# Kernel tuning notes

Hardware: AMD Instinct MI355X
Metric: run time of the kernel (lower is better)

## Reference

```python
import jax, jax.numpy as jnp
import numpy as np

T, I, H, O, M = 1024, 128, 512, 512, 32768
BETA = 8.0


def setup_inputs() -> dict:
    key = jax.random.key(0)
    ks = jax.random.split(key, 8)
    s = 0.05  # small init scale to keep tanh unsaturated
    return {
        "inp": jax.random.normal(ks[0], (T, I), jnp.float32),
        "x_obs": jax.nn.softmax(jax.random.normal(ks[1], (T, O), jnp.float32), axis=-1),
        "patterns": jax.random.normal(ks[2], (M, O + H), jnp.float32),  # stored [x | g] slots
        "last_hidden": jnp.zeros((H,), jnp.float32),
        "W_ih": jax.random.normal(ks[3], (H, I), jnp.float32) * s,
        "W_hh": jax.random.normal(ks[4], (H, H), jnp.float32) * s,
        "b_ih": jax.random.normal(ks[5], (H,), jnp.float32) * s,
        "b_hh": jax.random.normal(ks[6], (H,), jnp.float32) * s,
    }


def _retrieve(query, keys, values, beta):
    # distance-based slot attention: softmax(-beta * ||q - k||^2) @ values
    # sqdist via the expanded form to avoid a [T, M, D] intermediate
    d = (jnp.sum(query * query, axis=-1, keepdims=True)
         + jnp.sum(keys * keys, axis=-1)[None, :]
         - 2.0 * query @ keys.T)  # [T, M]
    w = jax.nn.softmax(-beta * d, axis=-1)
    return w @ values  # [T, O]


def reference(inp, x_obs, patterns, last_hidden, W_ih, W_hh, b_ih, b_hh):
    # single-layer tanh RNN (nn.RNN semantics), unbatched [T, I]
    def step(h, x):
        h_new = jnp.tanh(x @ W_ih.T + b_ih + h @ W_hh.T + b_hh)
        return h_new, h_new

    h_last, g_cur = jax.lax.scan(step, last_hidden, inp)  # g_cur: [T, H]

    x_vals = patterns[:, :O]   # stored x-parts
    g_keys = patterns[:, O:]   # stored g-parts
    prob_g = _retrieve(g_cur, g_keys, x_vals, BETA)   # index_g=True
    prob_x = _retrieve(x_obs, x_vals, x_vals, BETA)   # index_g=False
    # memory.store(hstack([x_obs, g_cur])) is a pure side effect on the buffer
    # and does not affect this step's outputs.
    return prob_g, prob_x, g_cur, h_last[None, :]
```

## Files before the change

kernel.cpp:

```cpp
#include <hip/hip_runtime.h>
#include <math.h>

#define T_STEPS 1024
#define I_DIM   128
#define H_DIM   512
#define O_DIM   512
#define M_PAT   32768
#define SCAN_ROLES 32
#define VT_STR  32800

typedef __attribute__((ext_vector_type(8))) short s16x8;
typedef __attribute__((ext_vector_type(4))) float f32x4;

__device__ __forceinline__ void bf_split(float f, unsigned short& hi, unsigned short& lo) {
  unsigned u = __builtin_bit_cast(unsigned, f);
  hi = (unsigned short)(u >> 16);
  float r = f - __builtin_bit_cast(float, u & 0xFFFF0000u);
  lo = (unsigned short)(__builtin_bit_cast(unsigned, r) >> 16);
}
__device__ __forceinline__ unsigned short f2bf(float f) {
  return (unsigned short)(__builtin_bit_cast(unsigned, f) >> 16);
}
__device__ __forceinline__ float bf2f(unsigned short b) {
  return __builtin_bit_cast(float, ((unsigned)b) << 16);
}

__global__ __launch_bounds__(256) void xw_kernel(const float* __restrict__ inp,
    const float* __restrict__ W_ih, const float* __restrict__ b_ih,
    const float* __restrict__ b_hh, float* __restrict__ xw) {
  int t = blockIdx.x;
  __shared__ float4 xs4[I_DIM / 4];
  if (threadIdx.x < I_DIM / 4)
    xs4[threadIdx.x] = ((const float4*)(inp + (size_t)t * I_DIM))[threadIdx.x];
  __syncthreads();
  for (int j = threadIdx.x; j < H_DIM; j += 256) {
    const float4* w4 = (const float4*)(W_ih + (size_t)j * I_DIM);
    float acc = 0.f;
#pragma unroll
    for (int i = 0; i < I_DIM / 4; i++) {
      float4 w = w4[i]; float4 x = xs4[i];
      acc += w.x * x.x + w.y * x.y + w.z * x.z + w.w * x.w;
    }
    xw[(size_t)t * H_DIM + j] = acc + b_ih[j] + b_hh[j];
  }
}

__global__ __launch_bounds__(64, 1) void scan_kernel(
    const float* __restrict__ W_hh, const float* __restrict__ xw,
    const float* __restrict__ h0, float* __restrict__ g_cur,
    float* __restrict__ h_last, unsigned* __restrict__ sync,
    unsigned* __restrict__ henc) {
  unsigned* cnt  = sync + 64;
  unsigned* dec  = sync + 128;
  __shared__ int role_s;
  if (threadIdx.x == 0) {
    unsigned xcd = __builtin_amdgcn_s_getreg(6164) & 7u;
    unsigned my_idx = __hip_atomic_fetch_add(&cnt[xcd], 1u, __ATOMIC_ACQ_REL,
                                             __HIP_MEMORY_SCOPE_AGENT);
    if (blockIdx.x == 0) {
      int chosen = -1;
      while (chosen < 0) {
        for (int x = 0; x < 8; x++)
          if (__hip_atomic_load(&cnt[x], __ATOMIC_ACQUIRE,
                                __HIP_MEMORY_SCOPE_AGENT) >= (unsigned)SCAN_ROLES) {
            chosen = x; break;
          }
        if (chosen < 0) __builtin_amdgcn_s_sleep(2);
      }
      __hip_atomic_store(dec, 1u + (unsigned)chosen, __ATOMIC_RELEASE,
                         __HIP_MEMORY_SCOPE_AGENT);
    }
    unsigned d;
    while ((d = __hip_atomic_load(dec, __ATOMIC_ACQUIRE,
                                  __HIP_MEMORY_SCOPE_AGENT)) == 0u)
      __builtin_amdgcn_s_sleep(2);
    role_s = (xcd == d - 1u && my_idx < (unsigned)SCAN_ROLES) ? (int)my_idx : -1;
  }
  __syncthreads();
  const int role = role_s;
  if (role < 0) return;

  const int lane = threadIdx.x;
  const int g    = lane & 3;
  const int row  = role * 16 + (lane >> 2);

  float4 w[32];
  const float4* wsrc = (const float4*)(W_hh + (size_t)row * H_DIM + g * 128);
#pragma unroll
  for (int i = 0; i < 32; i++) w[i] = wsrc[i];
#pragma unroll
  for (int i = 0; i < 32; i++) {
    asm volatile("" : "+v"(w[i].x), "+v"(w[i].y), "+v"(w[i].z), "+v"(w[i].w));
  }

  __shared__ float hbuf[528];

  float xw_next = xw[row];

  for (int t = 0; t < T_STEPS; t++) {
    float xwv = xw_next;
    if (t + 1 < T_STEPS)
      xw_next = xw[(size_t)(t + 1) * H_DIM + row];

    if (t == 0) {
#pragma unroll
      for (int j = 0; j < 8; j++) {
        int c = 64 * j + lane;
        hbuf[c + 4 * (j >> 1)] = h0[c];
      }
    } else {
      const unsigned* src = henc + (size_t)(t - 1) * H_DIM;
      unsigned u[8];
#pragma unroll
      for (int j = 0; j < 8; j++)
        u[j] = __hip_atomic_load(src + 64 * j + lane, __ATOMIC_RELAXED,
                                 __HIP_MEMORY_SCOPE_AGENT);
      bool again = true;
      while (again) {
        again = false;
#pragma unroll
        for (int j = 0; j < 8; j++)
          if (__builtin_bit_cast(float, u[j]) < 1.0f) {
            again = true;
            u[j] = __hip_atomic_load(src + 64 * j + lane, __ATOMIC_RELAXED,
                                     __HIP_MEMORY_SCOPE_AGENT);
          }
      }
#pragma unroll
      for (int j = 0; j < 8; j++) {
        int c = 64 * j + lane;
        hbuf[c + 4 * (j >> 1)] = __builtin_bit_cast(float, u[j]) - 2.0f;
      }
    }
    asm volatile("s_waitcnt lgkmcnt(0)" ::: "memory");

    const float4* hb = (const float4*)&hbuf[g * 132];
    float a0 = 0.f, a1 = 0.f, a2 = 0.f, a3 = 0.f;
#pragma unroll
    for (int i = 0; i < 8; i++) {
      float4 x0 = hb[4 * i], x1 = hb[4 * i + 1], x2 = hb[4 * i + 2], x3 = hb[4 * i + 3];
      float4 w0 = w[4 * i], w1 = w[4 * i + 1], w2 = w[4 * i + 2], w3 = w[4 * i + 3];
      a0 += x0.x * w0.x + x0.y * w0.y + x0.z * w0.z + x0.w * w0.w;
      a1 += x1.x * w1.x + x1.y * w1.y + x1.z * w1.z + x1.w * w1.w;
      a2 += x2.x * w2.x + x2.y * w2.y + x2.z * w2.z + x2.w * w2.w;
      a3 += x3.x * w3.x + x3.y * w3.y + x3.z * w3.z + x3.w * w3.w;
    }
    float a = (a0 + a1) + (a2 + a3);
    a += __shfl_xor(a, 1, 4);
    a += __shfl_xor(a, 2, 4);

    if (g == 0) {
      float pre = a + xwv;
      float e = __expf(2.f * pre);
      float h = 1.f - 2.f / (e + 1.f);
      __hip_atomic_store(henc + (size_t)t * H_DIM + row,
                         __builtin_bit_cast(unsigned, h + 2.0f),
                         __ATOMIC_RELAXED, __HIP_MEMORY_SCOPE_AGENT);
      g_cur[(size_t)t * H_DIM + row] = h;
      if (t == T_STEPS - 1) h_last[row] = h;
    }
  }
}

__global__ __launch_bounds__(256) void norms_kernel(const float* __restrict__ patterns,
    float* __restrict__ bkx, float* __restrict__ bkg) {
  int lane = threadIdx.x & 63;
  int m = blockIdx.x * 4 + (threadIdx.x >> 6);
  const float4* row = (const float4*)(patterns + (size_t)m * (O_DIM + H_DIM));
  float ax = 0.f, ag = 0.f;
#pragma unroll
  for (int jj = 0; jj < 4; jj++) {
    float4 v = row[lane + 64 * jj];
    float s = v.x * v.x + v.y * v.y + v.z * v.z + v.w * v.w;
    if (jj < 2) ax += s; else ag += s;
  }
#pragma unroll
  for (int off = 1; off < 64; off <<= 1) {
    ax += __shfl_xor(ax, off, 64);
    ag += __shfl_xor(ag, off, 64);
  }
  if (lane == 0) { bkx[m] = 8.f * ax; bkg[m] = 8.f * ag; }
}

__global__ __launch_bounds__(256) void vt_kernel(const float* __restrict__ patterns,
                                                 unsigned short* __restrict__ Vt) {
  __shared__ unsigned short tile[64 * 68];
  int kt = blockIdx.x;
  int vt = blockIdx.y;
#pragma unroll
  for (int i = 0; i < 4; i++) {
    int f = threadIdx.x + 256 * i;
    int key = f >> 4, c4 = f & 15;
    float4 v = *(const float4*)(patterns + (size_t)(kt * 64 + key) * 1024 + vt * 64 + c4 * 4);
    unsigned short* dst = &tile[key * 68 + c4 * 4];
    dst[0] = f2bf(v.x); dst[1] = f2bf(v.y); dst[2] = f2bf(v.z); dst[3] = f2bf(v.w);
  }
  __syncthreads();
  int vd = threadIdx.x >> 2, q4 = threadIdx.x & 3;
  unsigned short tmp[16];
#pragma unroll
  for (int k = 0; k < 16; k++) tmp[k] = tile[(q4 * 16 + k) * 68 + vd];
  size_t ob = (size_t)(vt * 64 + vd) * VT_STR + kt * 64 + q4 * 16;
#pragma unroll
  for (int h = 0; h < 2; h++) {
    s16x8 pk;
#pragma unroll
    for (int j = 0; j < 8; j++) pk[j] = (short)tmp[h * 8 + j];
    *(s16x8*)&Vt[ob + h * 8] = pk;
  }
}

template <bool USE_VT>
__global__ __launch_bounds__(512, 2) void flash_kernel(
    const float* __restrict__ Qg, const float* __restrict__ Qx,
    const float* __restrict__ patterns, const float* __restrict__ bkx,
    const float* __restrict__ bkg, const unsigned short* __restrict__ Vt,
    float* __restrict__ pacc, float* __restrict__ pml, int S) {
  const int bid  = blockIdx.x;
  const int sidx = bid >> 6;
  const int ret  = (bid >> 5) & 1;
  const int qt   = bid & 31;
  const int qbase = qt * 32;

  const float* Qp  = ret ? Qx : Qg;
  const float* Kp  = patterns + (ret ? 0 : O_DIM);
  const float* bkk = ret ? bkx : bkg;

  const int chunk = M_PAT / S;
  const int kbeg = sidx * chunk, kend = kbeg + chunk;

  const int lane = threadIdx.x & 63;
  const int wid  = threadIdx.x >> 6;
  const int qg   = wid >> 2;
  const int kw   = wid & 3;
  const int quad = lane >> 4;
  const int l16  = lane & 15;

  __shared__ unsigned short stage_u16[16384];
  __shared__ unsigned short p_lds[32 * 72];
  __shared__ float mrow_s[32], lrow_s[32], alpha_s[32];
  __shared__ int flag_s;

  const int qrow = qbase + qg * 16 + l16;
  s16x8 qhi[16], qlo[16];
#pragma unroll
  for (int kst = 0; kst < 16; kst++) {
    const float4* src = (const float4*)(Qp + (size_t)qrow * 512 + kst * 32 + quad * 8);
    float4 a = src[0], b = src[1];
    float fv[8] = {a.x, a.y, a.z, a.w, b.x, b.y, b.z, b.w};
    s16x8 h, l;
#pragma unroll
    for (int j = 0; j < 8; j++) {
      unsigned short hb, lb; bf_split(fv[j], hb, lb);
      h[j] = (short)hb; l[j] = (short)lb;
    }
    qhi[kst] = h; qlo[kst] = l;
  }

  if (threadIdx.x < 32) { mrow_s[threadIdx.x] = -INFINITY; lrow_s[threadIdx.x] = 0.f; }

  f32x4 o[8];
#pragma unroll
  for (int nb = 0; nb < 8; nb++) o[nb] = (f32x4){0.f, 0.f, 0.f, 0.f};
  float ov[32];
  if (!USE_VT) {
#pragma unroll
    for (int j = 0; j < 32; j++) ov[j] = 0.f;
  }
  const int row2 = threadIdx.x >> 4;
  const int c0   = threadIdx.x & 15;

  for (int k0 = kbeg; k0 < kend; k0 += 64) {
    f32x4 sc = (f32x4){0.f, 0.f, 0.f, 0.f};
#pragma unroll
    for (int dc = 0; dc < 4; dc++) {
      __syncthreads();
      if (dc == 0 && threadIdx.x == 0) flag_s = 0;
#pragma unroll
      for (int i = 0; i < 2; i++) {
        int oid = threadIdx.x + 512 * i;
        int key = oid >> 4, oct = oid & 15;
        const float4* src = (const float4*)(Kp + (size_t)(k0 + key) * 1024 + dc * 128 + oct * 8);
        float4 a = src[0], b = src[1];
        float fv[8] = {a.x, a.y, a.z, a.w, b.x, b.y, b.z, b.w};
        s16x8 hv, lv;
#pragma unroll
        for (int j = 0; j < 8; j++) {
          unsigned short hb, lb; bf_split(fv[j], hb, lb);
          hv[j] = (short)hb; lv[j] = (short)lb;
        }
        int base = (key * 16 + (oct ^ (key & 7))) * 8;
        *(s16x8*)&stage_u16[base] = hv;
        *(s16x8*)&stage_u16[8192 + base] = lv;
      }
      __syncthreads();
#pragma unroll
      for (int ks = 0; ks < 4; ks++) {
        int kst = dc * 4 + ks;
        int key = kw * 16 + l16;
        int oct = ks * 4 + quad;
        int base = (key * 16 + (oct ^ (key & 7))) * 8;
        s16x8 kh = *(const s16x8*)&stage_u16[base];
        s16x8 kl = *(const s16x8*)&stage_u16[8192 + base];
        sc = __builtin_amdgcn_mfma_f32_16x16x32_bf16(qhi[kst], kh, sc, 0, 0, 0);
        sc = __builtin_amdgcn_mfma_f32_16x16x32_bf16(qlo[kst], kh, sc, 0, 0, 0);
        sc = __builtin_amdgcn_mfma_f32_16x16x32_bf16(qhi[kst], kl, sc, 0, 0, 0);
      }
    }
    float bkv = bkk[k0 + kw * 16 + l16];
    __syncthreads();
    float* S_f = (float*)stage_u16;
#pragma unroll
    for (int r = 0; r < 4; r++)
      S_f[(qg * 16 + quad * 4 + r) * 68 + kw * 16 + l16] = 16.f * sc[r] - bkv;
    __syncthreads();

    float s4[4], p4[4];
#pragma unroll
    for (int c = 0; c < 4; c++) s4[c] = S_f[row2 * 68 + c0 + 16 * c];
    float tmax = fmaxf(fmaxf(s4[0], s4[1]), fmaxf(s4[2], s4[3]));
#pragma unroll
    for (int off = 1; off < 16; off <<= 1) tmax = fmaxf(tmax, __shfl_xor(tmax, off, 16));
    float mold = mrow_s[row2];
    float mnew = fmaxf(mold, tmax);
    float tsum = 0.f;
#pragma unroll
    for (int c = 0; c < 4; c++) { p4[c] = __expf(s4[c] - mnew); tsum += p4[c]; }
#pragma unroll
    for (int off = 1; off < 16; off <<= 1) tsum += __shfl_xor(tsum, off, 16);
#pragma unroll
    for (int c = 0; c < 4; c++) p_lds[row2 * 72 + c0 + 16 * c] = f2bf(p4[c]);
    if (c0 == 0) {
      float al = __expf(mold - mnew);
      alpha_s[row2] = al;
      mrow_s[row2] = mnew;
      lrow_s[row2] = lrow_s[row2] * al + tsum;
      if (tmax > mold - 25.f) flag_s = 1;
    }
    __syncthreads();
    const int doPV = flag_s;

    if (doPV) {
      if (USE_VT) {
        float alr[4];
#pragma unroll
        for (int r = 0; r < 4; r++) alr[r] = alpha_s[qg * 16 + quad * 4 + r];
#pragma unroll
        for (int nb = 0; nb < 8; nb++) {
          o[nb][0] *= alr[0]; o[nb][1] *= alr[1]; o[nb][2] *= alr[2]; o[nb][3] *= alr[3];
        }
#pragma unroll
        for (int ks2 = 0; ks2 < 2; ks2++) {
          s16x8 pf = *(const s16x8*)&p_lds[(qg * 16 + l16) * 72 + ks2 * 32 + quad * 8];
#pragma unroll
          for (int nb = 0; nb < 8; nb++) {
            int vd = kw * 128 + nb * 16 + l16;
            s16x8 vf = *(const s16x8*)(Vt + (size_t)vd * VT_STR + (k0 + ks2 * 32 + quad * 8));
            o[nb] = __builtin_amdgcn_mfma_f32_16x16x32_bf16(pf, vf, o[nb], 0, 0, 0);
          }
        }
      } else {
        float al = alpha_s[row2];
#pragma unroll
        for (int j = 0; j < 32; j++) ov[j] *= al;
        for (int key = 0; key < 64; key++) {
          float w = bf2f(p_lds[row2 * 72 + key]);
          const float4* vsrc = (const float4*)(patterns + (size_t)(k0 + key) * 1024 + c0 * 32);
#pragma unroll
          for (int j = 0; j < 8; j++) {
            float4 v = vsrc[j];
            ov[4 * j + 0] += w * v.x; ov[4 * j + 1] += w * v.y;
            ov[4 * j + 2] += w * v.z; ov[4 * j + 3] += w * v.w;
          }
        }
      }
    }
  }

  __syncthreads();
  size_t pbase = ((size_t)(ret * S + sidx) * T_STEPS + qbase);
  if (USE_VT) {
#pragma unroll
    for (int nb = 0; nb < 8; nb++)
#pragma unroll
      for (int r = 0; r < 4; r++)
        pacc[(pbase + qg * 16 + quad * 4 + r) * 512 + kw * 128 + nb * 16 + l16] = o[nb][r];
  } else {
#pragma unroll
    for (int j = 0; j < 32; j++)
      pacc[(pbase + row2) * 512 + c0 * 32 + j] = ov[j];
  }
  if (threadIdx.x < 32) {
    pml[(pbase + threadIdx.x) * 2]     = mrow_s[threadIdx.x];
    pml[(pbase + threadIdx.x) * 2 + 1] = lrow_s[threadIdx.x];
  }
}

__global__ __launch_bounds__(256) void combine_kernel(
    const float* __restrict__ pacc, const float* __restrict__ pml,
    float* __restrict__ out, int S) {
  int b = blockIdx.x;
  int ret = b >> 10, r = b & 1023;
  float M = -INFINITY;
  for (int s = 0; s < S; s++)
    M = fmaxf(M, pml[((size_t)(ret * S + s) * T_STEPS + r) * 2]);
  float L = 0.f;
  for (int s = 0; s < S; s++) {
    size_t mb = ((size_t)(ret * S + s) * T_STEPS + r) * 2;
    L += pml[mb + 1] * __expf(pml[mb] - M);
  }
  float inv = 1.0f / L;
  for (int cc = threadIdx.x; cc < 512; cc += 256) {
    float acc = 0.f;
    for (int s = 0; s < S; s++) {
      size_t mb = ((size_t)(ret * S + s) * T_STEPS + r) * 2;
      float sc = __expf(pml[mb] - M);
      acc += sc * pacc[((size_t)(ret * S + s) * T_STEPS + r) * 512 + cc];
    }
    out[(size_t)ret * (T_STEPS * O_DIM) + (size_t)r * 512 + cc] = acc * inv;
  }
}

extern "C" void kernel_launch(void* const* d_in, const int* in_sizes, int n_in,
                              void* d_out, int out_size, void* d_ws, size_t ws_size,
                              hipStream_t stream) {
  const float* inp      = (const float*)d_in[0];
  const float* x_obs    = (const float*)d_in[1];
  const float* patterns = (const float*)d_in[2];
  const float* h0       = (const float*)d_in[3];
  const float* W_ih     = (const float*)d_in[4];
  const float* W_hh     = (const float*)d_in[5];
  const float* b_ih     = (const float*)d_in[6];
  const float* b_hh     = (const float*)d_in[7];

  float* out    = (float*)d_out;
  float* g_cur  = out + 1048576;
  float* h_last = out + 1572864;

  char* wsb = (char*)d_ws;
  size_t off = 0;
  auto alloc = [&](size_t bytes) -> char* {
    char* p = wsb + off; off += (bytes + 255) & ~(size_t)255; return p;
  };
  unsigned* sync = (unsigned*)alloc(8192);
  unsigned* henc = (unsigned*)alloc((size_t)T_STEPS * H_DIM * 4);
  float* xw  = (float*)alloc((size_t)T_STEPS * H_DIM * 4);
  float* bkx = (float*)alloc((size_t)M_PAT * 4);
  float* bkg = (float*)alloc((size_t)M_PAT * 4);
  size_t base = off;

  const size_t vt_bytes = (size_t)512 * VT_STR * 2;
  auto pml_bytes  = [](int S) { return (size_t)2 * S * T_STEPS * 2 * 4; };
  auto pacc_bytes = [](int S) { return (size_t)2 * S * T_STEPS * 512 * 4; };

  int S = 4; bool use_vt = false;
  if (base + pml_bytes(4) + pacc_bytes(4) + vt_bytes + 1024 <= ws_size) { S = 4; use_vt = true; }
  else if (base + pml_bytes(2) + pacc_bytes(2) + vt_bytes + 1024 <= ws_size) { S = 2; use_vt = true; }
  else if (base + pml_bytes(4) + pacc_bytes(4) + 1024 <= ws_size) { S = 4; use_vt = false; }
  else if (base + pml_bytes(2) + pacc_bytes(2) + 1024 <= ws_size) { S = 2; use_vt = false; }
  else { S = 1; use_vt = false; }

  float* pml  = (float*)alloc(pml_bytes(S));
  float* pacc = (float*)alloc(pacc_bytes(S));
  unsigned short* Vt = use_vt ? (unsigned short*)alloc(vt_bytes) : (unsigned short*)nullptr;

  hipMemsetAsync(sync, 0, 8192, stream);
  hipMemsetAsync(henc, 0, (size_t)T_STEPS * H_DIM * 4, stream);
  xw_kernel<<<T_STEPS, 256, 0, stream>>>(inp, W_ih, b_ih, b_hh, xw);
  scan_kernel<<<1024, 64, 0, stream>>>(W_hh, xw, h0, g_cur, h_last, sync, henc);
  norms_kernel<<<M_PAT / 4, 256, 0, stream>>>(patterns, bkx, bkg);
  if (use_vt) {
    vt_kernel<<<dim3(512, 8), 256, 0, stream>>>(patterns, Vt);
    flash_kernel<true><<<S * 64, 512, 0, stream>>>(g_cur, x_obs, patterns, bkx, bkg,
                                                   Vt, pacc, pml, S);
  } else {
    flash_kernel<false><<<S * 64, 512, 0, stream>>>(g_cur, x_obs, patterns, bkx, bkg,
                                                    nullptr, pacc, pml, S);
  }
  combine_kernel<<<2 * T_STEPS, 256, 0, stream>>>(pacc, pml, out, S);
}
```

Measured before the change: 2.624 ms.

## Fuse RNN scan with flash retrieval so attention overlaps the recurrence

Merges the scan kernel and the flash retrieval kernel into one persistent launch. The 32 scan workgroups run on one XCD, while the other workgroups pull work units from an atomic counter. x_obs retrieval units come first, and g units spin on the per-row henc readiness flags before they start. The goal is to hide the serial recurrence latency behind the independent attention work. The change also raises the key-split count S to as much as 16 for finer-grained units. The risks are spin-waiting that occupies compute units, larger combine and partial buffers, and possible contention between the flash waves and the latency-critical scan waves on the shared XCD.

```diff
diff --git a/kernel.cpp b/kernel.cpp
--- a/kernel.cpp
+++ b/kernel.cpp
@@ -45,14 +45,76 @@
   }
 }
 
-__global__ __launch_bounds__(64, 1) void scan_kernel(
+__global__ __launch_bounds__(256) void norms_kernel(const float* __restrict__ patterns,
+    float* __restrict__ bkx, float* __restrict__ bkg) {
+  int lane = threadIdx.x & 63;
+  int m = blockIdx.x * 4 + (threadIdx.x >> 6);
+  const float4* row = (const float4*)(patterns + (size_t)m * (O_DIM + H_DIM));
+  float ax = 0.f, ag = 0.f;
+#pragma unroll
+  for (int jj = 0; jj < 4; jj++) {
+    float4 v = row[lane + 64 * jj];
+    float s = v.x * v.x + v.y * v.y + v.z * v.z + v.w * v.w;
+    if (jj < 2) ax += s; else ag += s;
+  }
+#pragma unroll
+  for (int off = 1; off < 64; off <<= 1) {
+    ax += __shfl_xor(ax, off, 64);
+    ag += __shfl_xor(ag, off, 64);
+  }
+  if (lane == 0) { bkx[m] = 8.f * ax; bkg[m] = 8.f * ag; }
+}
+
+__global__ __launch_bounds__(256) void vt_kernel(const float* __restrict__ patterns,
+                                                 unsigned short* __restrict__ Vt) {
+  __shared__ unsigned short tile[64 * 68];
+  int kt = blockIdx.x;
+  int vt = blockIdx.y;
+#pragma unroll
+  for (int i = 0; i < 4; i++) {
+    int f = threadIdx.x + 256 * i;
+    int key = f >> 4, c4 = f & 15;
+    float4 v = *(const float4*)(patterns + (size_t)(kt * 64 + key) * 1024 + vt * 64 + c4 * 4);
+    unsigned short* dst = &tile[key * 68 + c4 * 4];
+    dst[0] = f2bf(v.x); dst[1] = f2bf(v.y); dst[2] = f2bf(v.z); dst[3] = f2bf(v.w);
+  }
+  __syncthreads();
+  int vd = threadIdx.x >> 2, q4 = threadIdx.x & 3;
+  unsigned short tmp[16];
+#pragma unroll
+  for (int k = 0; k < 16; k++) tmp[k] = tile[(q4 * 16 + k) * 68 + vd];
+  size_t ob = (size_t)(vt * 64 + vd) * VT_STR + kt * 64 + q4 * 16;
+#pragma unroll
+  for (int h = 0; h < 2; h++) {
+    s16x8 pk;
+#pragma unroll
+    for (int j = 0; j < 8; j++) pk[j] = (short)tmp[h * 8 + j];
+    *(s16x8*)&Vt[ob + h * 8] = pk;
+  }
+}
+
+template <bool USE_VT>
+__global__ __launch_bounds__(512, 2) void fused_kernel(
     const float* __restrict__ W_hh, const float* __restrict__ xw,
     const float* __restrict__ h0, float* __restrict__ g_cur,
     float* __restrict__ h_last, unsigned* __restrict__ sync,
-    unsigned* __restrict__ henc) {
+    unsigned* __restrict__ henc,
+    const float* __restrict__ Qx, const float* __restrict__ patterns,
+    const float* __restrict__ bkx, const float* __restrict__ bkg,
+    const unsigned short* __restrict__ Vt,
+    float* __restrict__ pacc, float* __restrict__ pml, int S) {
   unsigned* cnt  = sync + 64;
   unsigned* dec  = sync + 128;
+  unsigned* wctr = sync + 192;
+
   __shared__ int role_s;
+  __shared__ float hbuf[528];
+  __shared__ unsigned short stage_u16[16384];
+  __shared__ unsigned short p_lds[32 * 72];
+  __shared__ float mrow_s[32], lrow_s[32], alpha_s[32];
+  __shared__ int flag_s;
+  __shared__ int unit_s;
+
   if (threadIdx.x == 0) {
     unsigned xcd = __builtin_amdgcn_s_getreg(6164) & 7u;
     unsigned my_idx = __hip_atomic_fetch_add(&cnt[xcd], 1u, __ATOMIC_ACQ_REL,
@@ -74,160 +136,95 @@
     while ((d = __hip_atomic_load(dec, __ATOMIC_ACQUIRE,
                                   __HIP_MEMORY_SCOPE_AGENT)) == 0u)
       __builtin_amdgcn_s_sleep(2);
-    role_s = (xcd == d - 1u && my_idx < (unsigned)SCAN_ROLES) ? (int)my_idx : -1;
+    if (xcd == d - 1u) role_s = (my_idx < (unsigned)SCAN_ROLES) ? (int)my_idx : -2;
+    else               role_s = -1;
   }
   __syncthreads();
   const int role = role_s;
-  if (role < 0) return;
-
-  const int lane = threadIdx.x;
-  const int g    = lane & 3;
-  const int row  = role * 16 + (lane >> 2);
-
-  float4 w[32];
-  const float4* wsrc = (const float4*)(W_hh + (size_t)row * H_DIM + g * 128);
-#pragma unroll
-  for (int i = 0; i < 32; i++) w[i] = wsrc[i];
-#pragma unroll
-  for (int i = 0; i < 32; i++) {
-    asm volatile("" : "+v"(w[i].x), "+v"(w[i].y), "+v"(w[i].z), "+v"(w[i].w));
-  }
-
-  __shared__ float hbuf[528];
-
-  float xw_next = xw[row];
-
-  for (int t = 0; t < T_STEPS; t++) {
-    float xwv = xw_next;
-    if (t + 1 < T_STEPS)
-      xw_next = xw[(size_t)(t + 1) * H_DIM + row];
-
-    if (t == 0) {
-#pragma unroll
-      for (int j = 0; j < 8; j++) {
-        int c = 64 * j + lane;
-        hbuf[c + 4 * (j >> 1)] = h0[c];
-      }
-    } else {
-      const unsigned* src = henc + (size_t)(t - 1) * H_DIM;
-      unsigned u[8];
-#pragma unroll
-      for (int j = 0; j < 8; j++)
-        u[j] = __hip_atomic_load(src + 64 * j + lane, __ATOMIC_RELAXED,
-                                 __HIP_MEMORY_SCOPE_AGENT);
-      bool again = true;
-      while (again) {
-        again = false;
+  if (role == -2) return;
+
+  if (role >= 0) {
+    if (threadIdx.x >= 64) return;
+    const int lane = threadIdx.x;
+    const int g    = lane & 3;
+    const int row  = role * 16 + (lane >> 2);
+
+    float4 w[32];
+    const float4* wsrc = (const float4*)(W_hh + (size_t)row * H_DIM + g * 128);
+#pragma unroll
+    for (int i = 0; i < 32; i++) w[i] = wsrc[i];
+#pragma unroll
+    for (int i = 0; i < 32; i++) {
+      asm volatile("" : "+v"(w[i].x), "+v"(w[i].y), "+v"(w[i].z), "+v"(w[i].w));
+    }
+
+    float xw_next = xw[row];
+
+    for (int t = 0; t < T_STEPS; t++) {
+      float xwv = xw_next;
+      if (t + 1 < T_STEPS)
+        xw_next = xw[(size_t)(t + 1) * H_DIM + row];
+
+      if (t == 0) {
+#pragma unroll
+        for (int j = 0; j < 8; j++) {
+          int c = 64 * j + lane;
+          hbuf[c + 4 * (j >> 1)] = h0[c];
+        }
+      } else {
+        const unsigned* src = henc + (size_t)(t - 1) * H_DIM;
+        unsigned u[8];
 #pragma unroll
         for (int j = 0; j < 8; j++)
-          if (__builtin_bit_cast(float, u[j]) < 1.0f) {
-            again = true;
-            u[j] = __hip_atomic_load(src + 64 * j + lane, __ATOMIC_RELAXED,
-                                     __HIP_MEMORY_SCOPE_AGENT);
-          }
-      }
-#pragma unroll
-      for (int j = 0; j < 8; j++) {
-        int c = 64 * j + lane;
-        hbuf[c + 4 * (j >> 1)] = __builtin_bit_cast(float, u[j]) - 2.0f;
-      }
-    }
-    asm volatile("s_waitcnt lgkmcnt(0)" ::: "memory");
-
-    const float4* hb = (const float4*)&hbuf[g * 132];
-    float a0 = 0.f, a1 = 0.f, a2 = 0.f, a3 = 0.f;
-#pragma unroll
-    for (int i = 0; i < 8; i++) {
-      float4 x0 = hb[4 * i], x1 = hb[4 * i + 1], x2 = hb[4 * i + 2], x3 = hb[4 * i + 3];
-      float4 w0 = w[4 * i], w1 = w[4 * i + 1], w2 = w[4 * i + 2], w3 = w[4 * i + 3];
-      a0 += x0.x * w0.x + x0.y * w0.y + x0.z * w0.z + x0.w * w0.w;
-      a1 += x1.x * w1.x + x1.y * w1.y + x1.z * w1.z + x1.w * w1.w;
-      a2 += x2.x * w2.x + x2.y * w2.y + x2.z * w2.z + x2.w * w2.w;
-      a3 += x3.x * w3.x + x3.y * w3.y + x3.z * w3.z + x3.w * w3.w;
-    }
-    float a = (a0 + a1) + (a2 + a3);
-    a += __shfl_xor(a, 1, 4);
-    a += __shfl_xor(a, 2, 4);
-
-    if (g == 0) {
-      float pre = a + xwv;
-      float e = __expf(2.f * pre);
-      float h = 1.f - 2.f / (e + 1.f);
-      __hip_atomic_store(henc + (size_t)t * H_DIM + row,
-                         __builtin_bit_cast(unsigned, h + 2.0f),
-                         __ATOMIC_RELAXED, __HIP_MEMORY_SCOPE_AGENT);
-      g_cur[(size_t)t * H_DIM + row] = h;
-      if (t == T_STEPS - 1) h_last[row] = h;
-    }
-  }
-}
-
-__global__ __launch_bounds__(256) void norms_kernel(const float* __restrict__ patterns,
-    float* __restrict__ bkx, float* __restrict__ bkg) {
-  int lane = threadIdx.x & 63;
-  int m = blockIdx.x * 4 + (threadIdx.x >> 6);
-  const float4* row = (const float4*)(patterns + (size_t)m * (O_DIM + H_DIM));
-  float ax = 0.f, ag = 0.f;
-#pragma unroll
-  for (int jj = 0; jj < 4; jj++) {
-    float4 v = row[lane + 64 * jj];
-    float s = v.x * v.x + v.y * v.y + v.z * v.z + v.w * v.w;
-    if (jj < 2) ax += s; else ag += s;
-  }
-#pragma unroll
-  for (int off = 1; off < 64; off <<= 1) {
-    ax += __shfl_xor(ax, off, 64);
-    ag += __shfl_xor(ag, off, 64);
-  }
-  if (lane == 0) { bkx[m] = 8.f * ax; bkg[m] = 8.f * ag; }
-}
-
-__global__ __launch_bounds__(256) void vt_kernel(const float* __restrict__ patterns,
-                                                 unsigned short* __restrict__ Vt) {
-  __shared__ unsigned short tile[64 * 68];
-  int kt = blockIdx.x;
-  int vt = blockIdx.y;
-#pragma unroll
-  for (int i = 0; i < 4; i++) {
-    int f = threadIdx.x + 256 * i;
-    int key = f >> 4, c4 = f & 15;
-    float4 v = *(const float4*)(patterns + (size_t)(kt * 64 + key) * 1024 + vt * 64 + c4 * 4);
-    unsigned short* dst = &tile[key * 68 + c4 * 4];
-    dst[0] = f2bf(v.x); dst[1] = f2bf(v.y); dst[2] = f2bf(v.z); dst[3] = f2bf(v.w);
-  }
-  __syncthreads();
-  int vd = threadIdx.x >> 2, q4 = threadIdx.x & 3;
-  unsigned short tmp[16];
-#pragma unroll
-  for (int k = 0; k < 16; k++) tmp[k] = tile[(q4 * 16 + k) * 68 + vd];
-  size_t ob = (size_t)(vt * 64 + vd) * VT_STR + kt * 64 + q4 * 16;
-#pragma unroll
-  for (int h = 0; h < 2; h++) {
-    s16x8 pk;
-#pragma unroll
-    for (int j = 0; j < 8; j++) pk[j] = (short)tmp[h * 8 + j];
-    *(s16x8*)&Vt[ob + h * 8] = pk;
-  }
-}
-
-template <bool USE_VT>
-__global__ __launch_bounds__(512, 2) void flash_kernel(
-    const float* __restrict__ Qg, const float* __restrict__ Qx,
-    const float* __restrict__ patterns, const float* __restrict__ bkx,
-    const float* __restrict__ bkg, const unsigned short* __restrict__ Vt,
-    float* __restrict__ pacc, float* __restrict__ pml, int S) {
-  const int bid  = blockIdx.x;
-  const int sidx = bid >> 6;
-  const int ret  = (bid >> 5) & 1;
-  const int qt   = bid & 31;
-  const int qbase = qt * 32;
-
-  const float* Qp  = ret ? Qx : Qg;
-  const float* Kp  = patterns + (ret ? 0 : O_DIM);
-  const float* bkk = ret ? bkx : bkg;
-
-  const int chunk = M_PAT / S;
-  const int kbeg = sidx * chunk, kend = kbeg + chunk;
+          u[j] = __hip_atomic_load(src + 64 * j + lane, __ATOMIC_RELAXED,
+                                   __HIP_MEMORY_SCOPE_AGENT);
+        bool again = true;
+        while (again) {
+          again = false;
+#pragma unroll
+          for (int j = 0; j < 8; j++)
+            if (__builtin_bit_cast(float, u[j]) < 1.0f) {
+              again = true;
+              u[j] = __hip_atomic_load(src + 64 * j + lane, __ATOMIC_RELAXED,
+                                       __HIP_MEMORY_SCOPE_AGENT);
+            }
+        }
+#pragma unroll
+        for (int j = 0; j < 8; j++) {
+          int c = 64 * j + lane;
+          hbuf[c + 4 * (j >> 1)] = __builtin_bit_cast(float, u[j]) - 2.0f;
+        }
+      }
+      asm volatile("s_waitcnt lgkmcnt(0)" ::: "memory");
+
+      const float4* hb = (const float4*)&hbuf[g * 132];
+      float a0 = 0.f, a1 = 0.f, a2 = 0.f, a3 = 0.f;
+#pragma unroll
+      for (int i = 0; i < 8; i++) {
+        float4 x0 = hb[4 * i], x1 = hb[4 * i + 1], x2 = hb[4 * i + 2], x3 = hb[4 * i + 3];
+        float4 w0 = w[4 * i], w1 = w[4 * i + 1], w2 = w[4 * i + 2], w3 = w[4 * i + 3];
+        a0 += x0.x * w0.x + x0.y * w0.y + x0.z * w0.z + x0.w * w0.w;
+        a1 += x1.x * w1.x + x1.y * w1.y + x1.z * w1.z + x1.w * w1.w;
+        a2 += x2.x * w2.x + x2.y * w2.y + x2.z * w2.z + x2.w * w2.w;
+        a3 += x3.x * w3.x + x3.y * w3.y + x3.z * w3.z + x3.w * w3.w;
+      }
+      float a = (a0 + a1) + (a2 + a3);
+      a += __shfl_xor(a, 1, 4);
+      a += __shfl_xor(a, 2, 4);
+
+      if (g == 0) {
+        float pre = a + xwv;
+        float e = __expf(2.f * pre);
+        float h = 1.f - 2.f / (e + 1.f);
+        __hip_atomic_store(henc + (size_t)t * H_DIM + row,
+                           __builtin_bit_cast(unsigned, h + 2.0f),
+                           __ATOMIC_RELAXED, __HIP_MEMORY_SCOPE_AGENT);
+        g_cur[(size_t)t * H_DIM + row] = h;
+        if (t == T_STEPS - 1) h_last[row] = h;
+      }
+    }
+    return;
+  }
 
   const int lane = threadIdx.x & 63;
   const int wid  = threadIdx.x >> 6;
@@ -235,164 +232,197 @@
   const int kw   = wid & 3;
   const int quad = lane >> 4;
   const int l16  = lane & 15;
-
-  __shared__ unsigned short stage_u16[16384];
-  __shared__ unsigned short p_lds[32 * 72];
-  __shared__ float mrow_s[32], lrow_s[32], alpha_s[32];
-  __shared__ int flag_s;
-
-  const int qrow = qbase + qg * 16 + l16;
-  s16x8 qhi[16], qlo[16];
-#pragma unroll
-  for (int kst = 0; kst < 16; kst++) {
-    const float4* src = (const float4*)(Qp + (size_t)qrow * 512 + kst * 32 + quad * 8);
-    float4 a = src[0], b = src[1];
-    float fv[8] = {a.x, a.y, a.z, a.w, b.x, b.y, b.z, b.w};
-    s16x8 h, l;
-#pragma unroll
-    for (int j = 0; j < 8; j++) {
-      unsigned short hb, lb; bf_split(fv[j], hb, lb);
-      h[j] = (short)hb; l[j] = (short)lb;
-    }
-    qhi[kst] = h; qlo[kst] = l;
-  }
-
-  if (threadIdx.x < 32) { mrow_s[threadIdx.x] = -INFINITY; lrow_s[threadIdx.x] = 0.f; }
-
-  f32x4 o[8];
-#pragma unroll
-  for (int nb = 0; nb < 8; nb++) o[nb] = (f32x4){0.f, 0.f, 0.f, 0.f};
-  float ov[32];
-  if (!USE_VT) {
-#pragma unroll
-    for (int j = 0; j < 32; j++) ov[j] = 0.f;
-  }
   const int row2 = threadIdx.x >> 4;
   const int c0   = threadIdx.x & 15;
-
-  for (int k0 = kbeg; k0 < kend; k0 += 64) {
-    f32x4 sc = (f32x4){0.f, 0.f, 0.f, 0.f};
-#pragma unroll
-    for (int dc = 0; dc < 4; dc++) {
+  const int NU   = 64 * S;
+
+  for (;;) {
+    if (threadIdx.x == 0)
+      unit_s = (int)__hip_atomic_fetch_add(wctr, 1u, __ATOMIC_RELAXED,
+                                           __HIP_MEMORY_SCOPE_AGENT);
+    __syncthreads();
+    const int u = unit_s;
+    if (u >= NU) break;
+
+    int ret, qt, sidx;
+    if (u < 32 * S) { ret = 1; qt = u & 31; sidx = u >> 5; }
+    else { int v = u - 32 * S; qt = v / S; sidx = v - qt * S; ret = 0; }
+    const int qbase = qt * 32;
+
+    const float* Kp  = patterns + (ret ? 0 : O_DIM);
+    const float* bkk = ret ? bkx : bkg;
+    const int chunk = M_PAT / S;
+    const int kbeg = sidx * chunk, kend = kbeg + chunk;
+
+    const int qrow = qbase + qg * 16 + l16;
+    s16x8 qhi[16], qlo[16];
+#pragma unroll
+    for (int kst = 0; kst < 16; kst++) {
+      float fv[8];
+      if (ret) {
+        const float4* src = (const float4*)(Qx + (size_t)qrow * 512 + kst * 32 + quad * 8);
+        float4 a = src[0], b = src[1];
+        fv[0] = a.x; fv[1] = a.y; fv[2] = a.z; fv[3] = a.w;
+        fv[4] = b.x; fv[5] = b.y; fv[6] = b.z; fv[7] = b.w;
+      } else {
+        const unsigned* hs = henc + (size_t)qrow * H_DIM + kst * 32 + quad * 8;
+#pragma unroll
+        for (int j = 0; j < 8; j++) {
+          unsigned uv = __hip_atomic_load(hs + j, __ATOMIC_RELAXED,
+                                          __HIP_MEMORY_SCOPE_AGENT);
+          while (__builtin_bit_cast(float, uv) < 1.0f) {
+            __builtin_amdgcn_s_sleep(8);
+            uv = __hip_atomic_load(hs + j, __ATOMIC_RELAXED,
+                                   __HIP_MEMORY_SCOPE_AGENT);
+          }
+          fv[j] = __builtin_bit_cast(float, uv) - 2.0f;
+        }
+      }
+      s16x8 h, l;
+#pragma unroll
+      for (int j = 0; j < 8; j++) {
+        unsigned short hb, lb; bf_split(fv[j], hb, lb);
+        h[j] = (short)hb; l[j] = (short)lb;
+      }
+      qhi[kst] = h; qlo[kst] = l;
+    }
+
+    if (threadIdx.x < 32) { mrow_s[threadIdx.x] = -INFINITY; lrow_s[threadIdx.x] = 0.f; }
+
+    f32x4 o[8];
+#pragma unroll
+    for (int nb = 0; nb < 8; nb++) o[nb] = (f32x4){0.f, 0.f, 0.f, 0.f};
+    float ov[32];
+    if (!USE_VT) {
+#pragma unroll
+      for (int j = 0; j < 32; j++) ov[j] = 0.f;
+    }
+
+    for (int k0 = kbeg; k0 < kend; k0 += 64) {
+      f32x4 sc = (f32x4){0.f, 0.f, 0.f, 0.f};
+#pragma unroll
+      for (int dc = 0; dc < 4; dc++) {
+        __syncthreads();
+        if (dc == 0 && threadIdx.x == 0) flag_s = 0;
+#pragma unroll
+        for (int i = 0; i < 2; i++) {
+          int oid = threadIdx.x + 512 * i;
+          int key = oid >> 4, oct = oid & 15;
+          const float4* src = (const float4*)(Kp + (size_t)(k0 + key) * 1024 + dc * 128 + oct * 8);
+          float4 a = src[0], b = src[1];
+          float fv[8] = {a.x, a.y, a.z, a.w, b.x, b.y, b.z, b.w};
+          s16x8 hv, lv;
+#pragma unroll
+          for (int j = 0; j < 8; j++) {
+            unsigned short hb, lb; bf_split(fv[j], hb, lb);
+            hv[j] = (short)hb; lv[j] = (short)lb;
+          }
+          int base = (key * 16 + (oct ^ (key & 7))) * 8;
+          *(s16x8*)&stage_u16[base] = hv;
+          *(s16x8*)&stage_u16[8192 + base] = lv;
+        }
+        __syncthreads();
+#pragma unroll
+        for (int ks = 0; ks < 4; ks++) {
+          int kst = dc * 4 + ks;
+          int key = kw * 16 + l16;
+          int oct = ks * 4 + quad;
+          int base = (key * 16 + (oct ^ (key & 7))) * 8;
+          s16x8 kh = *(const s16x8*)&stage_u16[base];
+          s16x8 kl = *(const s16x8*)&stage_u16[8192 + base];
+          sc = __builtin_amdgcn_mfma_f32_16x16x32_bf16(qhi[kst], kh, sc, 0, 0, 0);
+          sc = __builtin_amdgcn_mfma_f32_16x16x32_bf16(qlo[kst], kh, sc, 0, 0, 0);
+          sc = __builtin_amdgcn_mfma_f32_16x16x32_bf16(qhi[kst], kl, sc, 0, 0, 0);
+        }
+      }
+      float bkv = bkk[k0 + kw * 16 + l16];
       __syncthreads();
-      if (dc == 0 && threadIdx.x == 0) flag_s = 0;
-#pragma unroll
-      for (int i = 0; i < 2; i++) {
-        int oid = threadIdx.x + 512 * i;
-        int key = oid >> 4, oct = oid & 15;
-        const float4* src = (const float4*)(Kp + (size_t)(k0 + key) * 1024 + dc * 128 + oct * 8);
-        float4 a = src[0], b = src[1];
-        float fv[8] = {a.x, a.y, a.z, a.w, b.x, b.y, b.z, b.w};
-        s16x8 hv, lv;
-#pragma unroll
-        for (int j = 0; j < 8; j++) {
-          unsigned short hb, lb; bf_split(fv[j], hb, lb);
-          hv[j] = (short)hb; lv[j] = (short)lb;
-        }
-        int base = (key * 16 + (oct ^ (key & 7))) * 8;
-        *(s16x8*)&stage_u16[base] = hv;
-        *(s16x8*)&stage_u16[8192 + base] = lv;
-      }
+      float* S_f = (float*)stage_u16;
+#pragma unroll
+      for (int r = 0; r < 4; r++)
+        S_f[(qg * 16 + quad * 4 + r) * 68 + kw * 16 + l16] = 16.f * sc[r] - bkv;
       __syncthreads();
-#pragma unroll
-      for (int ks = 0; ks < 4; ks++) {
-        int kst = dc * 4 + ks;
-        int key = kw * 16 + l16;
-        int oct = ks * 4 + quad;
-        int base = (key * 16 + (oct ^ (key & 7))) * 8;
-        s16x8 kh = *(const s16x8*)&stage_u16[base];
-        s16x8 kl = *(const s16x8*)&stage_u16[8192 + base];
-        sc = __builtin_amdgcn_mfma_f32_16x16x32_bf16(qhi[kst], kh, sc, 0, 0, 0);
-        sc = __builtin_amdgcn_mfma_f32_16x16x32_bf16(qlo[kst], kh, sc, 0, 0, 0);
-        sc = __builtin_amdgcn_mfma_f32_16x16x32_bf16(qhi[kst], kl, sc, 0, 0, 0);
-      }
-    }
-    float bkv = bkk[k0 + kw * 16 + l16];
+
+      float s4[4], p4[4];
+#pragma unroll
+      for (int c = 0; c < 4; c++) s4[c] = S_f[row2 * 68 + c0 + 16 * c];
+      float tmax = fmaxf(fmaxf(s4[0], s4[1]), fmaxf(s4[2], s4[3]));
+#pragma unroll
+      for (int off = 1; off < 16; off <<= 1) tmax = fmaxf(tmax, __shfl_xor(tmax, off, 16));
+      float mold = mrow_s[row2];
+      float mnew = fmaxf(mold, tmax);
+      float tsum = 0.f;
+#pragma unroll
+      for (int c = 0; c < 4; c++) { p4[c] = __expf(s4[c] - mnew); tsum += p4[c]; }
+#pragma unroll
+      for (int off = 1; off < 16; off <<= 1) tsum += __shfl_xor(tsum, off, 16);
+#pragma unroll
+      for (int c = 0; c < 4; c++) p_lds[row2 * 72 + c0 + 16 * c] = f2bf(p4[c]);
+      if (c0 == 0) {
+        float al = __expf(mold - mnew);
+        alpha_s[row2] = al;
+        mrow_s[row2] = mnew;
+        lrow_s[row2] = lrow_s[row2] * al + tsum;
+        if (tmax > mold - 25.f) flag_s = 1;
+      }
+      __syncthreads();
+      const int doPV = flag_s;
+
+      if (doPV) {
+        if (USE_VT) {
+          float alr[4];
+#pragma unroll
+          for (int r = 0; r < 4; r++) alr[r] = alpha_s[qg * 16 + quad * 4 + r];
+#pragma unroll
+          for (int nb = 0; nb < 8; nb++) {
+            o[nb][0] *= alr[0]; o[nb][1] *= alr[1]; o[nb][2] *= alr[2]; o[nb][3] *= alr[3];
+          }
+#pragma unroll
+          for (int ks2 = 0; ks2 < 2; ks2++) {
+            s16x8 pf = *(const s16x8*)&p_lds[(qg * 16 + l16) * 72 + ks2 * 32 + quad * 8];
+#pragma unroll
+            for (int nb = 0; nb < 8; nb++) {
+              int vd = kw * 128 + nb * 16 + l16;
+              s16x8 vf = *(const s16x8*)(Vt + (size_t)vd * VT_STR + (k0 + ks2 * 32 + quad * 8));
+              o[nb] = __builtin_amdgcn_mfma_f32_16x16x32_bf16(pf, vf, o[nb], 0, 0, 0);
+            }
+          }
+        } else {
+          float al = alpha_s[row2];
+#pragma unroll
+          for (int j = 0; j < 32; j++) ov[j] *= al;
+          for (int key = 0; key < 64; key++) {
+            float w = bf2f(p_lds[row2 * 72 + key]);
+            const float4* vsrc = (const float4*)(patterns + (size_t)(k0 + key) * 1024 + c0 * 32);
+#pragma unroll
+            for (int j = 0; j < 8; j++) {
+              float4 v = vsrc[j];
+              ov[4 * j + 0] += w * v.x; ov[4 * j + 1] += w * v.y;
+              ov[4 * j + 2] += w * v.z; ov[4 * j + 3] += w * v.w;
+            }
+          }
+        }
+      }
+    }
+
     __syncthreads();
-    float* S_f = (float*)stage_u16;
-#pragma unroll
-    for (int r = 0; r < 4; r++)
-      S_f[(qg * 16 + quad * 4 + r) * 68 + kw * 16 + l16] = 16.f * sc[r] - bkv;
+    size_t pbase = ((size_t)(ret * S + sidx) * T_STEPS + qbase);
+    if (USE_VT) {
+#pragma unroll
+      for (int nb = 0; nb < 8; nb++)
+#pragma unroll
+        for (int r = 0; r < 4; r++)
+          pacc[(pbase + qg * 16 + quad * 4 + r) * 512 + kw * 128 + nb * 16 + l16] = o[nb][r];
+    } else {
+#pragma unroll
+      for (int j = 0; j < 32; j++)
+        pacc[(pbase + row2) * 512 + c0 * 32 + j] = ov[j];
+    }
+    if (threadIdx.x < 32) {
+      pml[(pbase + threadIdx.x) * 2]     = mrow_s[threadIdx.x];
+      pml[(pbase + threadIdx.x) * 2 + 1] = lrow_s[threadIdx.x];
+    }
     __syncthreads();
-
-    float s4[4], p4[4];
-#pragma unroll
-    for (int c = 0; c < 4; c++) s4[c] = S_f[row2 * 68 + c0 + 16 * c];
-    float tmax = fmaxf(fmaxf(s4[0], s4[1]), fmaxf(s4[2], s4[3]));
-#pragma unroll
-    for (int off = 1; off < 16; off <<= 1) tmax = fmaxf(tmax, __shfl_xor(tmax, off, 16));
-    float mold = mrow_s[row2];
-    float mnew = fmaxf(mold, tmax);
-    float tsum = 0.f;
-#pragma unroll
-    for (int c = 0; c < 4; c++) { p4[c] = __expf(s4[c] - mnew); tsum += p4[c]; }
-#pragma unroll
-    for (int off = 1; off < 16; off <<= 1) tsum += __shfl_xor(tsum, off, 16);
-#pragma unroll
-    for (int c = 0; c < 4; c++) p_lds[row2 * 72 + c0 + 16 * c] = f2bf(p4[c]);
-    if (c0 == 0) {
-      float al = __expf(mold - mnew);
-      alpha_s[row2] = al;
-      mrow_s[row2] = mnew;
-      lrow_s[row2] = lrow_s[row2] * al + tsum;
-      if (tmax > mold - 25.f) flag_s = 1;
-    }
-    __syncthreads();
-    const int doPV = flag_s;
-
-    if (doPV) {
-      if (USE_VT) {
-        float alr[4];
-#pragma unroll
-        for (int r = 0; r < 4; r++) alr[r] = alpha_s[qg * 16 + quad * 4 + r];
-#pragma unroll
-        for (int nb = 0; nb < 8; nb++) {
-          o[nb][0] *= alr[0]; o[nb][1] *= alr[1]; o[nb][2] *= alr[2]; o[nb][3] *= alr[3];
-        }
-#pragma unroll
-        for (int ks2 = 0; ks2 < 2; ks2++) {
-          s16x8 pf = *(const s16x8*)&p_lds[(qg * 16 + l16) * 72 + ks2 * 32 + quad * 8];
-#pragma unroll
-          for (int nb = 0; nb < 8; nb++) {
-            int vd = kw * 128 + nb * 16 + l16;
-            s16x8 vf = *(const s16x8*)(Vt + (size_t)vd * VT_STR + (k0 + ks2 * 32 + quad * 8));
-            o[nb] = __builtin_amdgcn_mfma_f32_16x16x32_bf16(pf, vf, o[nb], 0, 0, 0);
-          }
-        }
-      } else {
-        float al = alpha_s[row2];
-#pragma unroll
-        for (int j = 0; j < 32; j++) ov[j] *= al;
-        for (int key = 0; key < 64; key++) {
-          float w = bf2f(p_lds[row2 * 72 + key]);
-          const float4* vsrc = (const float4*)(patterns + (size_t)(k0 + key) * 1024 + c0 * 32);
-#pragma unroll
-          for (int j = 0; j < 8; j++) {
-            float4 v = vsrc[j];
-            ov[4 * j + 0] += w * v.x; ov[4 * j + 1] += w * v.y;
-            ov[4 * j + 2] += w * v.z; ov[4 * j + 3] += w * v.w;
-          }
-        }
-      }
-    }
-  }
-
-  __syncthreads();
-  size_t pbase = ((size_t)(ret * S + sidx) * T_STEPS + qbase);
-  if (USE_VT) {
-#pragma unroll
-    for (int nb = 0; nb < 8; nb++)
-#pragma unroll
-      for (int r = 0; r < 4; r++)
-        pacc[(pbase + qg * 16 + quad * 4 + r) * 512 + kw * 128 + nb * 16 + l16] = o[nb][r];
-  } else {
-#pragma unroll
-    for (int j = 0; j < 32; j++)
-      pacc[(pbase + row2) * 512 + c0 * 32 + j] = ov[j];
-  }
-  if (threadIdx.x < 32) {
-    pml[(pbase + threadIdx.x) * 2]     = mrow_s[threadIdx.x];
-    pml[(pbase + threadIdx.x) * 2 + 1] = lrow_s[threadIdx.x];
   }
 }
 
@@ -454,10 +484,12 @@
   auto pacc_bytes = [](int S) { return (size_t)2 * S * T_STEPS * 512 * 4; };
 
   int S = 4; bool use_vt = false;
-  if (base + pml_bytes(4) + pacc_bytes(4) + vt_bytes + 1024 <= ws_size) { S = 4; use_vt = true; }
-  else if (base + pml_bytes(2) + pacc_bytes(2) + vt_bytes + 1024 <= ws_size) { S = 2; use_vt = true; }
-  else if (base + pml_bytes(4) + pacc_bytes(4) + 1024 <= ws_size) { S = 4; use_vt = false; }
-  else if (base + pml_bytes(2) + pacc_bytes(2) + 1024 <= ws_size) { S = 2; use_vt = false; }
+  if      (base + pml_bytes(16) + pacc_bytes(16) + vt_bytes + 1024 <= ws_size) { S = 16; use_vt = true; }
+  else if (base + pml_bytes(8)  + pacc_bytes(8)  + vt_bytes + 1024 <= ws_size) { S = 8;  use_vt = true; }
+  else if (base + pml_bytes(4)  + pacc_bytes(4)  + vt_bytes + 1024 <= ws_size) { S = 4;  use_vt = true; }
+  else if (base + pml_bytes(2)  + pacc_bytes(2)  + vt_bytes + 1024 <= ws_size) { S = 2;  use_vt = true; }
+  else if (base + pml_bytes(4)  + pacc_bytes(4)  + 1024 <= ws_size)            { S = 4;  use_vt = false; }
+  else if (base + pml_bytes(2)  + pacc_bytes(2)  + 1024 <= ws_size)            { S = 2;  use_vt = false; }
   else { S = 1; use_vt = false; }
 
   float* pml  = (float*)alloc(pml_bytes(S));
@@ -467,15 +499,14 @@
   hipMemsetAsync(sync, 0, 8192, stream);
   hipMemsetAsync(henc, 0, (size_t)T_STEPS * H_DIM * 4, stream);
   xw_kernel<<<T_STEPS, 256, 0, stream>>>(inp, W_ih, b_ih, b_hh, xw);
-  scan_kernel<<<1024, 64, 0, stream>>>(W_hh, xw, h0, g_cur, h_last, sync, henc);
   norms_kernel<<<M_PAT / 4, 256, 0, stream>>>(patterns, bkx, bkg);
   if (use_vt) {
     vt_kernel<<<dim3(512, 8), 256, 0, stream>>>(patterns, Vt);
-    flash_kernel<true><<<S * 64, 512, 0, stream>>>(g_cur, x_obs, patterns, bkx, bkg,
-                                                   Vt, pacc, pml, S);
+    fused_kernel<true><<<1024, 512, 0, stream>>>(W_hh, xw, h0, g_cur, h_last, sync, henc,
+                                                 x_obs, patterns, bkx, bkg, Vt, pacc, pml, S);
   } else {
-    flash_kernel<false><<<S * 64, 512, 0, stream>>>(g_cur, x_obs, patterns, bkx, bkg,
-                                                    nullptr, pacc, pml, S);
+    fused_kernel<false><<<1024, 512, 0, stream>>>(W_hh, xw, h0, g_cur, h_last, sync, henc,
+                                                  x_obs, patterns, bkx, bkg, nullptr, pacc, pml, S);
   }
   combine_kernel<<<2 * T_STEPS, 256, 0, stream>>>(pacc, pml, out, S);
 }
```

Result: faster. 2.181 ms (-16.9%).
